# Kernel optimization log

Measured on AMD Instinct MI355X. Metric: run time of the kernel, lower is better.

The kernel has to match this reference:

```python
import jax, jax.numpy as jnp
import numpy as np

SENT_LEN, SENT_BATCH, WORD_LEN = 256, 64, 16
EMB, HID = 128, 256
CEMB, CHID = 64, 128
VOCAB, CVOCAB, TAGS = 50000, 128, 50


def setup_inputs() -> dict:
    key = jax.random.key(0)
    ks = jax.random.split(key, 14)
    s = 0.1  # param init scale, avoids gate saturation
    n = lambda k, shape: (jax.random.normal(k, shape, dtype=jnp.float32) * s)
    return {
        "sentences": jax.random.randint(ks[0], (SENT_LEN, SENT_BATCH), 0, VOCAB),
        "words": jax.random.randint(ks[1], (SENT_BATCH, WORD_LEN, SENT_LEN), 0, CVOCAB),
        "char_embedding_dim": CEMB,
        "char_hidden_dim": CHID,
        "word_emb": n(ks[2], (VOCAB, EMB)),
        "char_emb": n(ks[3], (CVOCAB, CEMB)),
        "Wih_c": n(ks[4], (4 * CHID, CEMB)),
        "Whh_c": n(ks[5], (4 * CHID, CHID)),
        "bih_c": n(ks[6], (4 * CHID,)),
        "bhh_c": n(ks[7], (4 * CHID,)),
        "Wih_w": n(ks[8], (4 * HID, EMB + CHID)),
        "Whh_w": n(ks[9], (4 * HID, HID)),
        "bih_w": n(ks[10], (4 * HID,)),
        "bhh_w": n(ks[11], (4 * HID,)),
        "W_tag": n(ks[12], (TAGS, HID)),
        "b_tag": n(ks[13], (TAGS,)),
    }


def _lstm_cell(h, c, x, Wih, Whh, b):
    # torch gate order: input, forget, cell(g), output
    gates = x @ Wih.T + h @ Whh.T + b
    i, f, g, o = jnp.split(gates, 4, axis=-1)
    c_new = jax.nn.sigmoid(f) * c + jax.nn.sigmoid(i) * jnp.tanh(g)
    h_new = jax.nn.sigmoid(o) * jnp.tanh(c_new)
    return h_new, c_new


def reference(sentences, words, char_embedding_dim, char_hidden_dim,
              word_emb, char_emb, Wih_c, Whh_c, bih_c, bhh_c,
              Wih_w, Whh_w, bih_w, bhh_w, W_tag, b_tag):
    sent_len, sent_batch = sentences.shape
    dt = word_emb.dtype

    embeds = word_emb[sentences]            # [T, B, EMB]
    ce = char_emb[words]                    # [B, WL, T, CEMB]

    # char LSTM: per sentence, seq=WL, batch=T; hidden carried ACROSS sentences
    b_c = bih_c + bhh_c

    def char_sentence(carry, sent_ce):      # sent_ce: [WL, T, CEMB]
        def step(hc, x):
            h, c = _lstm_cell(hc[0], hc[1], x, Wih_c, Whh_c, b_c)
            return (h, c), None
        carry, _ = jax.lax.scan(step, carry, sent_ce)
        return carry, carry[0]               # final h: [T, CHID]

    init_c = (jnp.zeros((sent_len, CHID), dt), jnp.zeros((sent_len, CHID), dt))
    _, char_finals = jax.lax.scan(char_sentence, init_c, ce)  # [B, T, CHID]
    char_finals = jnp.transpose(char_finals, (1, 0, 2))        # [T, B, CHID]

    x = jnp.concatenate([embeds, char_finals], axis=-1)        # [T, B, EMB+CHID]

    # word LSTM over time=T, batch=B
    b_w = bih_w + bhh_w

    def word_step(hc, xt):
        h, c = _lstm_cell(hc[0], hc[1], xt, Wih_w, Whh_w, b_w)
        return (h, c), h

    init_w = (jnp.zeros((sent_batch, HID), dt), jnp.zeros((sent_batch, HID), dt))
    _, lstm_out = jax.lax.scan(word_step, init_w, x)           # [T, B, HID]

    tag_space = lstm_out @ W_tag.T + b_tag                     # [T, B, TAGS]
    return jax.nn.log_softmax(tag_space, axis=-1)
```

## Files before the change

### kernel.cpp

```cpp
#include <hip/hip_runtime.h>
#include <hip/hip_bf16.h>
#include <cstdint>

#define SENT_LEN   256
#define SENT_BATCH 64
#define WORD_LEN   16
#define EMB        128
#define HID        256
#define CEMB       64
#define CHID       128
#define TAGS       50
#define K_IN       (EMB + CHID)
#define LOG2E      1.44269504f
#define N2LOG2E    -2.88539008f

typedef __attribute__((ext_vector_type(8))) short short8;
typedef __attribute__((ext_vector_type(4))) float f32x4;
typedef __attribute__((ext_vector_type(4))) int   i32x4;
typedef __attribute__((ext_vector_type(2))) long  lng2;

__device__ __forceinline__ float rcpf(float x) { return __builtin_amdgcn_rcpf(x); }
__device__ __forceinline__ float sig2(float xl) {
    return rcpf(1.f + __builtin_amdgcn_exp2f(-xl));
}
__device__ __forceinline__ float tanh2(float xl) {
    float e = __builtin_amdgcn_exp2f(-(xl + xl));
    return 2.f * rcpf(1.f + e) - 1.f;
}
__device__ __forceinline__ float lstm_act(float gi, float gf, float gg, float go, float& cst) {
    float c = sig2(gf) * cst + sig2(gi) * tanh2(gg);
    cst = c;
    float tc = 2.f * rcpf(1.f + __builtin_amdgcn_exp2f(N2LOG2E * c)) - 1.f;
    return sig2(go) * tc;
}
__device__ __forceinline__ float bf_lo(unsigned u) { return __uint_as_float(u << 16); }
__device__ __forceinline__ float bf_hi(unsigned u) { return __uint_as_float(u & 0xffff0000u); }
__device__ __forceinline__ unsigned short f2bfu(float f) {
    unsigned u = __float_as_uint(f);
    u += 0x7fff + ((u >> 16) & 1);
    return (unsigned short)(u >> 16);
}
__device__ __forceinline__ void block_sync_lds() {
    asm volatile("s_waitcnt lgkmcnt(0)\ns_barrier" ::: "memory");
}
__device__ __forceinline__ i32x4 mfma_i8_k64(lng2 a, lng2 b, i32x4 c) {
    c = __builtin_amdgcn_mfma_i32_16x16x32_i8(a.x, b.x, c, 0, 0, 0);
    return __builtin_amdgcn_mfma_i32_16x16x32_i8(a.y, b.y, c, 0, 0, 0);
}
template<int Q> __device__ __forceinline__ float qbcast(float x) {
    return __int_as_float(__builtin_amdgcn_mov_dpp(
        __float_as_int(x), Q * 0x55, 0xF, 0xF, false));
}

__global__ void prep_char(const float* __restrict__ Wih_c, const float* __restrict__ char_emb,
                          const float* __restrict__ bih_c, const float* __restrict__ bhh_c,
                          float* __restrict__ pre8) {
    int ch = blockIdx.x;
    int g  = threadIdx.x;
    float acc = bih_c[g] + bhh_c[g];
    const float* w = Wih_c + g * CEMB;
    const float* e = char_emb + ch * CEMB;
#pragma unroll
    for (int k = 0; k < CEMB; k++) acc += w[k] * e[k];
    int gt = g >> 7, j = g & 127;
    pre8[((ch * 128) + j) * 4 + gt] = acc * LOG2E;
}

__global__ void prep_wq(const float* __restrict__ Whh_w, signed char* __restrict__ wq,
                        float* __restrict__ sw) {
    int g = blockIdx.x;
    int lane = threadIdx.x;
    float4 v = reinterpret_cast<const float4*>(Whh_w + (size_t)g * HID)[lane];
    float m = fmaxf(fmaxf(fabsf(v.x), fabsf(v.y)), fmaxf(fabsf(v.z), fabsf(v.w)));
#pragma unroll
    for (int off = 32; off; off >>= 1) m = fmaxf(m, __shfl_xor(m, off, 64));
    m = fmaxf(m, 1e-20f);
    float inv = 127.f / m;
    int q0 = __float2int_rn(v.x * inv), q1 = __float2int_rn(v.y * inv);
    int q2 = __float2int_rn(v.z * inv), q3 = __float2int_rn(v.w * inv);
    int packed = (q0 & 255) | ((q1 & 255) << 8) | ((q2 & 255) << 16) | ((q3 & 255) << 24);
    reinterpret_cast<int*>(wq)[g * 64 + lane] = packed;
    if (lane == 0) sw[g] = m / 127.f;
}

__global__ __launch_bounds__(512, 1) void char_lstm(
        const int* __restrict__ words, const float* __restrict__ Whh_c,
        const float* __restrict__ pre8, float* __restrict__ cf) {
    int t    = blockIdx.x;
    int tid  = threadIdx.x;
    int lane = tid & 63, w = tid >> 6;
    int nt   = lane & 3;
    int j    = w * 16 + (lane >> 2);
    int g    = nt * 128 + j;

    __shared__ __align__(16) signed char hv[2][128];

    const float4* wr = reinterpret_cast<const float4*>(Whh_c + (size_t)g * CHID);
    float mx = 1e-20f;
#pragma unroll
    for (int q = 0; q < 32; q++) {
        float4 f = wr[q];
        mx = fmaxf(mx, fmaxf(fmaxf(fabsf(f.x), fabsf(f.y)), fmaxf(fabsf(f.z), fabsf(f.w))));
    }
    float inv = 127.f / mx;
    int wqr[32];
#pragma unroll
    for (int q = 0; q < 32; q++) {
        float4 f = wr[q];
        wqr[q] = (__float2int_rn(f.x * inv) & 255)
               | ((__float2int_rn(f.y * inv) & 255) << 8)
               | ((__float2int_rn(f.z * inv) & 255) << 16)
               | ((__float2int_rn(f.w * inv) & 255) << 24);
    }
    float swl = mx * (LOG2E / (127.f * 127.f));

    float s_e = (nt == 2) ? -2.f : -1.f;
    float m_a = (nt == 2) ?  2.f :  1.f;
    float b_a = (nt == 2) ? -1.f :  0.f;

    if (tid < 64) { reinterpret_cast<int*>(hv)[tid] = 0; }

    float cst = 0.f;
    int cid0 = words[t];
    int cid1 = words[SENT_LEN + t];
    float pl0 = pre8[(size_t)cid0 * 512 + tid];
    float pl1 = pre8[(size_t)cid1 * 512 + tid];
    int cidn0 = words[2 * SENT_LEN + t];
    int cidn1 = words[3 * SENT_LEN + t];
    __syncthreads();

    for (int u = 0; u < 512; u++) {
        float pn0 = pre8[(size_t)cidn0 * 512 + tid];
        float pn1 = pre8[(size_t)cidn1 * 512 + tid];
        cidn0 = words[(((u << 1) + 4) & 1023) * SENT_LEN + t];
        cidn1 = words[(((u << 1) + 5) & 1023) * SENT_LEN + t];

        {
            const i32x4* hp = reinterpret_cast<const i32x4*>(hv[0]);
            int a0 = 0, a1 = 0, a2 = 0, a3 = 0;
#pragma unroll
            for (int q = 0; q < 8; q++) {
                i32x4 hq = hp[q];
                a0 = __builtin_amdgcn_sdot4(hq.x, wqr[q * 4 + 0], a0, false);
                a1 = __builtin_amdgcn_sdot4(hq.y, wqr[q * 4 + 1], a1, false);
                a2 = __builtin_amdgcn_sdot4(hq.z, wqr[q * 4 + 2], a2, false);
                a3 = __builtin_amdgcn_sdot4(hq.w, wqr[q * 4 + 3], a3, false);
            }
            int acc = (a0 + a1) + (a2 + a3);
            float gv = (float)acc * swl + pl0;
            float e  = __builtin_amdgcn_exp2f(s_e * gv);
            float av = m_a * rcpf(1.f + e) + b_a;
            float qi = qbcast<0>(av);
            float qf = qbcast<1>(av);
            float qg = qbcast<2>(av);
            float qo = qbcast<3>(av);
            float c  = qf * cst + qi * qg;
            cst = c;
            float tc = 2.f * rcpf(1.f + __builtin_amdgcn_exp2f(N2LOG2E * c)) - 1.f;
            float h  = qo * tc;
            if (nt == 0)
                hv[1][j] = (signed char)__float2int_rn(h * 127.f);
            block_sync_lds();
        }
        {
            const i32x4* hp = reinterpret_cast<const i32x4*>(hv[1]);
            int a0 = 0, a1 = 0, a2 = 0, a3 = 0;
#pragma unroll
            for (int q = 0; q < 8; q++) {
                i32x4 hq = hp[q];
                a0 = __builtin_amdgcn_sdot4(hq.x, wqr[q * 4 + 0], a0, false);
                a1 = __builtin_amdgcn_sdot4(hq.y, wqr[q * 4 + 1], a1, false);
                a2 = __builtin_amdgcn_sdot4(hq.z, wqr[q * 4 + 2], a2, false);
                a3 = __builtin_amdgcn_sdot4(hq.w, wqr[q * 4 + 3], a3, false);
            }
            int acc = (a0 + a1) + (a2 + a3);
            float gv = (float)acc * swl + pl1;
            float e  = __builtin_amdgcn_exp2f(s_e * gv);
            float av = m_a * rcpf(1.f + e) + b_a;
            float qi = qbcast<0>(av);
            float qf = qbcast<1>(av);
            float qg = qbcast<2>(av);
            float qo = qbcast<3>(av);
            float c  = qf * cst + qi * qg;
            cst = c;
            float tc = 2.f * rcpf(1.f + __builtin_amdgcn_exp2f(N2LOG2E * c)) - 1.f;
            float h  = qo * tc;
            if (nt == 0) {
                hv[0][j] = (signed char)__float2int_rn(h * 127.f);
                if ((u & 7) == 7)
                    cf[((size_t)t * SENT_BATCH + (u >> 3)) * CHID + j] = h;
            }
            block_sync_lds();
        }
        pl0 = pn0; pl1 = pn1;
    }
}

#define XW_SEG 65
__global__ __launch_bounds__(256, 2) void xw_gemm(
        const int* __restrict__ sentences, const float* __restrict__ word_emb,
        const float* __restrict__ cf, const float* __restrict__ Wih_w,
        const float* __restrict__ bih_w, const float* __restrict__ bhh_w,
        uint2* __restrict__ xw8) {
    __shared__ short8 Apack[32 * XW_SEG];
    __shared__ short8 Bpack[32 * XW_SEG];
    __shared__ int sid_s[64];
    int tid = threadIdx.x;
    int j0 = blockIdx.x * 16;
    int row0 = blockIdx.y * 64;
    if (tid < 64) sid_s[tid] = sentences[row0 + tid];
    __syncthreads();

#pragma unroll
    for (int it = 0; it < 8; it++) {
        int idx = it * 256 + tid;
        int m = idx >> 5, k8 = idx & 31;
        int k = k8 * 8;
        int kt = k8 >> 2, lqs = k8 & 3;
        int lanes = (m & 15) + (lqs << 4);
        int seg = kt * 4 + (m >> 4);
        const float* asrc = (k < EMB)
            ? word_emb + (size_t)sid_s[m] * EMB + k
            : cf + (size_t)(row0 + m) * CHID + (k - EMB);
        float4 a0 = reinterpret_cast<const float4*>(asrc)[0];
        float4 a1 = reinterpret_cast<const float4*>(asrc)[1];
        short8 av;
        av[0] = (short)f2bfu(a0.x); av[1] = (short)f2bfu(a0.y);
        av[2] = (short)f2bfu(a0.z); av[3] = (short)f2bfu(a0.w);
        av[4] = (short)f2bfu(a1.x); av[5] = (short)f2bfu(a1.y);
        av[6] = (short)f2bfu(a1.z); av[7] = (short)f2bfu(a1.w);
        Apack[seg * XW_SEG + lanes] = av;
        const float* bsrc = Wih_w + (size_t)((m >> 4) * 256 + j0 + (m & 15)) * K_IN + k;
        float4 b0 = reinterpret_cast<const float4*>(bsrc)[0];
        float4 b1 = reinterpret_cast<const float4*>(bsrc)[1];
        short8 bv;
        bv[0] = (short)f2bfu(b0.x); bv[1] = (short)f2bfu(b0.y);
        bv[2] = (short)f2bfu(b0.z); bv[3] = (short)f2bfu(b0.w);
        bv[4] = (short)f2bfu(b1.x); bv[5] = (short)f2bfu(b1.y);
        bv[6] = (short)f2bfu(b1.z); bv[7] = (short)f2bfu(b1.w);
        Bpack[seg * XW_SEG + lanes] = bv;
    }
    __syncthreads();

    int lane = tid & 63, wv = tid >> 6, l15 = lane & 15, lq = lane >> 4;
    f32x4 acc[4] = {{0.f,0.f,0.f,0.f},{0.f,0.f,0.f,0.f},{0.f,0.f,0.f,0.f},{0.f,0.f,0.f,0.f}};
#pragma unroll
    for (int kt = 0; kt < 8; kt++) {
// ... 55 lines not shown
        uint2 xn0 = xwb[((((u << 1) + 4) & 255)) * 256 + j];
        uint2 xn1 = xwb[((((u << 1) + 5) & 255)) * 256 + j];

        {
            const lng2* hp = reinterpret_cast<const lng2*>(hv[0]);
            i32x4 acc[4] = {};
#pragma unroll
            for (int kt = 0; kt < 4; kt++) {
                lng2 a = hp[kt * 4 + lq];
#pragma unroll
                for (int nt = 0; nt < 4; nt++)
                    acc[nt] = mfma_i8_k64(a, bfr[nt][kt], acc[nt]);
            }
            float gi = (float)acc[0][0] * swl[0] + bf_lo(xq0.x);
            float gf = (float)acc[1][0] * swl[1] + bf_hi(xq0.x);
            float gg = (float)acc[2][0] * swl[2] + bf_lo(xq0.y);
            float go = (float)acc[3][0] * swl[3] + bf_hi(xq0.y);
            float h = lstm_act(gi, gf, gg, go, cst);
            if (lq == 0) {
                h_out[((size_t)(u << 1) * SENT_BATCH + b) * HID + j] = h;
                hv[1][j] = (signed char)__float2int_rn(h * 127.f);
            }
            block_sync_lds();
        }
        {
            const lng2* hp = reinterpret_cast<const lng2*>(hv[1]);
            i32x4 acc[4] = {};
#pragma unroll
            for (int kt = 0; kt < 4; kt++) {
                lng2 a = hp[kt * 4 + lq];
#pragma unroll
                for (int nt = 0; nt < 4; nt++)
                    acc[nt] = mfma_i8_k64(a, bfr[nt][kt], acc[nt]);
            }
            float gi = (float)acc[0][0] * swl[0] + bf_lo(xq1.x);
            float gf = (float)acc[1][0] * swl[1] + bf_hi(xq1.x);
            float gg = (float)acc[2][0] * swl[2] + bf_lo(xq1.y);
            float go = (float)acc[3][0] * swl[3] + bf_hi(xq1.y);
            float h = lstm_act(gi, gf, gg, go, cst);
            if (lq == 0) {
                h_out[((size_t)((u << 1) + 1) * SENT_BATCH + b) * HID + j] = h;
                hv[0][j] = (signed char)__float2int_rn(h * 127.f);
            }
            block_sync_lds();
        }
        xq0 = xq2; xq1 = xq3; xq2 = xn0; xq3 = xn1;
    }
}

__global__ __launch_bounds__(256) void tag_logsoftmax(
        const float* __restrict__ h_out, const float* __restrict__ W_tag,
        const float* __restrict__ b_tag, float* __restrict__ out) {
    __shared__ float wt_s[TAGS * 257];
    __shared__ float hr_s[4 * HID];
    int tid = threadIdx.x;
    int row0 = blockIdx.x * 4;
#pragma unroll 2
    for (int i = 0; i < TAGS; i++) wt_s[i * 257 + tid] = W_tag[i * HID + tid];
#pragma unroll
    for (int w = 0; w < 4; w++) hr_s[w * HID + tid] = h_out[(size_t)(row0 + w) * HID + tid];
    __syncthreads();

    int w = tid >> 6, l = tid & 63;
    float acc = 0.f;
    if (l < TAGS) {
        acc = b_tag[l];
        const float* hr = hr_s + w * HID;
        const float* wr = wt_s + l * 257;
#pragma unroll 4
        for (int k = 0; k < HID; k++) acc += hr[k] * wr[k];
    }
    float m = (l < TAGS) ? acc : -1e30f;
#pragma unroll
    for (int off = 32; off; off >>= 1) m = fmaxf(m, __shfl_xor(m, off, 64));
    float e = (l < TAGS) ? __builtin_amdgcn_exp2f((acc - m) * LOG2E) : 0.f;
    float ssum = e;
#pragma unroll
    for (int off = 32; off; off >>= 1) ssum += __shfl_xor(ssum, off, 64);
    float lse = m + __logf(ssum);
    if (l < TAGS) out[(size_t)(row0 + w) * TAGS + l] = acc - lse;
}

extern "C" void kernel_launch(void* const* d_in, const int* in_sizes, int n_in,
                              void* d_out, int out_size, void* d_ws, size_t ws_size,
                              hipStream_t stream) {
    (void)in_sizes; (void)n_in; (void)out_size; (void)ws_size;
    const int*   sentences = (const int*)d_in[0];
    const int*   words     = (const int*)d_in[1];
    const float* word_emb  = (const float*)d_in[4];
    const float* char_emb  = (const float*)d_in[5];
    const float* Wih_c     = (const float*)d_in[6];
    const float* Whh_c     = (const float*)d_in[7];
    const float* bih_c     = (const float*)d_in[8];
    const float* bhh_c     = (const float*)d_in[9];
    const float* Wih_w     = (const float*)d_in[10];
    const float* Whh_w     = (const float*)d_in[11];
    const float* bih_w     = (const float*)d_in[12];
    const float* bhh_w     = (const float*)d_in[13];
    const float* W_tag     = (const float*)d_in[14];
    const float* b_tag     = (const float*)d_in[15];
    float* out = (float*)d_out;

    char* ws = (char*)d_ws;
    size_t off = 0;
    float* pre8 = (float*)(ws + off);                 off += 128 * 512 * sizeof(float);
    signed char* wq = (signed char*)(ws + off);       off += 1024 * 256;
    float* sw = (float*)(ws + off);                   off += 1024 * sizeof(float);
    off = (off + 255) & ~(size_t)255;
    float* cf = (float*)(ws + off);                   off += (size_t)SENT_LEN * SENT_BATCH * CHID * sizeof(float);
    uint2* xw8 = (uint2*)(ws + off);                  off += (size_t)SENT_LEN * SENT_BATCH * 256 * sizeof(uint2);
    float* h_out = (float*)(ws + off);                off += (size_t)SENT_LEN * SENT_BATCH * HID * sizeof(float);

    hipLaunchKernelGGL(prep_char, dim3(128), dim3(512), 0, stream,
                       Wih_c, char_emb, bih_c, bhh_c, pre8);
    hipLaunchKernelGGL(prep_wq, dim3(1024), dim3(64), 0, stream, Whh_w, wq, sw);
    hipLaunchKernelGGL(char_lstm, dim3(256), dim3(512), 0, stream,
                       words, Whh_c, pre8, cf);
    hipLaunchKernelGGL(xw_gemm, dim3(16, 256), dim3(256), 0, stream,
                       sentences, word_emb, cf, Wih_w, bih_w, bhh_w, xw8);
    hipLaunchKernelGGL(word_lstm, dim3(SENT_BATCH), dim3(1024), 0, stream,
                       xw8, wq, sw, h_out);
    hipLaunchKernelGGL(tag_logsoftmax, dim3((SENT_LEN * SENT_BATCH) / 4), dim3(256), 0, stream,
                       h_out, W_tag, b_tag, out);
}
```

Measured before the change: 938.7 us.

## Process two independent char-LSTM chains per block to overlap latency

Each char_lstm block now runs two independent word positions (t0, t1) in an interleaved fashion, halving the grid from 256 to 128 blocks. This aims to hide the serial latency of each recurrent step (dot products, transcendental ops, LDS barrier) by giving the scheduler two independent dependency chains per barrier. The gate pre-activation scaling is also folded into prep_char and the sdot result so the inner step uses a single fma before exp2. Risk: fewer blocks means less use of the CUs, and the per-step work doubles, so the whole serial loop may end up longer if it was not latency-bound.

```diff
diff --git a/kernel.cpp b/kernel.cpp
--- a/kernel.cpp
+++ b/kernel.cpp
@@ -63,7 +63,8 @@
 #pragma unroll
     for (int k = 0; k < CEMB; k++) acc += w[k] * e[k];
     int gt = g >> 7, j = g & 127;
-    pre8[((ch * 128) + j) * 4 + gt] = acc * LOG2E;
+    float s_e = (gt == 2) ? -2.f : -1.f;
+    pre8[((ch * 128) + j) * 4 + gt] = acc * LOG2E * s_e;
 }
 
 __global__ void prep_wq(const float* __restrict__ Whh_w, signed char* __restrict__ wq,
@@ -86,14 +87,16 @@
 __global__ __launch_bounds__(512, 1) void char_lstm(
         const int* __restrict__ words, const float* __restrict__ Whh_c,
         const float* __restrict__ pre8, float* __restrict__ cf) {
-    int t    = blockIdx.x;
+    int bid  = blockIdx.x;
+    int t0   = bid * 2, t1 = bid * 2 + 1;
     int tid  = threadIdx.x;
     int lane = tid & 63, w = tid >> 6;
     int nt   = lane & 3;
     int j    = w * 16 + (lane >> 2);
     int g    = nt * 128 + j;
 
-    __shared__ __align__(16) signed char hv[2][128];
+    __shared__ __align__(16) signed char hv0[2][128];
+    __shared__ __align__(16) signed char hv1[2][128];
 
     const float4* wr = reinterpret_cast<const float4*>(Whh_c + (size_t)g * CHID);
     float mx = 1e-20f;
@@ -112,87 +115,129 @@
                | ((__float2int_rn(f.z * inv) & 255) << 16)
                | ((__float2int_rn(f.w * inv) & 255) << 24);
     }
-    float swl = mx * (LOG2E / (127.f * 127.f));
-
-    float s_e = (nt == 2) ? -2.f : -1.f;
-    float m_a = (nt == 2) ?  2.f :  1.f;
-    float b_a = (nt == 2) ? -1.f :  0.f;
-
-    if (tid < 64) { reinterpret_cast<int*>(hv)[tid] = 0; }
-
-    float cst = 0.f;
-    int cid0 = words[t];
-    int cid1 = words[SENT_LEN + t];
-    float pl0 = pre8[(size_t)cid0 * 512 + tid];
-    float pl1 = pre8[(size_t)cid1 * 512 + tid];
-    int cidn0 = words[2 * SENT_LEN + t];
-    int cidn1 = words[3 * SENT_LEN + t];
+    float s_e   = (nt == 2) ? -2.f : -1.f;
+    float swl_s = s_e * mx * (LOG2E / (127.f * 127.f));
+    float m_a   = (nt == 2) ?  2.f :  1.f;
+    float b_a   = (nt == 2) ? -1.f :  0.f;
+
+    if (tid < 64) { reinterpret_cast<int*>(hv0)[tid] = 0; reinterpret_cast<int*>(hv1)[tid] = 0; }
+
+    float cst0 = 0.f, cst1 = 0.f;
+    int   c0i2, c0i3, c1i2, c1i3;
+    float pc0, pn0, pc1, pn1;
+    {
+        int a0 = words[0 * SENT_LEN + t0], b0 = words[1 * SENT_LEN + t0];
+        int a1 = words[0 * SENT_LEN + t1], b1 = words[1 * SENT_LEN + t1];
+        pc0 = pre8[(size_t)a0 * 512 + tid];
+        pn0 = pre8[(size_t)b0 * 512 + tid];
+        pc1 = pre8[(size_t)a1 * 512 + tid];
+        pn1 = pre8[(size_t)b1 * 512 + tid];
+        c0i2 = words[2 * SENT_LEN + t0]; c0i3 = words[3 * SENT_LEN + t0];
+        c1i2 = words[2 * SENT_LEN + t1]; c1i3 = words[3 * SENT_LEN + t1];
+    }
     __syncthreads();
 
     for (int u = 0; u < 512; u++) {
-        float pn0 = pre8[(size_t)cidn0 * 512 + tid];
-        float pn1 = pre8[(size_t)cidn1 * 512 + tid];
-        cidn0 = words[(((u << 1) + 4) & 1023) * SENT_LEN + t];
-        cidn1 = words[(((u << 1) + 5) & 1023) * SENT_LEN + t];
-
         {
-            const i32x4* hp = reinterpret_cast<const i32x4*>(hv[0]);
+            float pf0 = pre8[(size_t)c0i2 * 512 + tid];
+            float pf1 = pre8[(size_t)c1i2 * 512 + tid];
+            int cn0 = words[(((u << 1) + 4) & 1023) * SENT_LEN + t0];
+            int cn1 = words[(((u << 1) + 4) & 1023) * SENT_LEN + t1];
+
+            const i32x4* h0p = reinterpret_cast<const i32x4*>(hv0[0]);
+            const i32x4* h1p = reinterpret_cast<const i32x4*>(hv1[0]);
             int a0 = 0, a1 = 0, a2 = 0, a3 = 0;
+            int b0 = 0, b1 = 0, b2 = 0, b3 = 0;
 #pragma unroll
             for (int q = 0; q < 8; q++) {
-                i32x4 hq = hp[q];
+                i32x4 hq = h0p[q];
                 a0 = __builtin_amdgcn_sdot4(hq.x, wqr[q * 4 + 0], a0, false);
                 a1 = __builtin_amdgcn_sdot4(hq.y, wqr[q * 4 + 1], a1, false);
                 a2 = __builtin_amdgcn_sdot4(hq.z, wqr[q * 4 + 2], a2, false);
                 a3 = __builtin_amdgcn_sdot4(hq.w, wqr[q * 4 + 3], a3, false);
             }
-            int acc = (a0 + a1) + (a2 + a3);
-            float gv = (float)acc * swl + pl0;
-            float e  = __builtin_amdgcn_exp2f(s_e * gv);
-            float av = m_a * rcpf(1.f + e) + b_a;
-            float qi = qbcast<0>(av);
-            float qf = qbcast<1>(av);
-            float qg = qbcast<2>(av);
-            float qo = qbcast<3>(av);
-            float c  = qf * cst + qi * qg;
-            cst = c;
-            float tc = 2.f * rcpf(1.f + __builtin_amdgcn_exp2f(N2LOG2E * c)) - 1.f;
-            float h  = qo * tc;
-            if (nt == 0)
-                hv[1][j] = (signed char)__float2int_rn(h * 127.f);
+#pragma unroll
+            for (int q = 0; q < 8; q++) {
+                i32x4 hq = h1p[q];
+                b0 = __builtin_amdgcn_sdot4(hq.x, wqr[q * 4 + 0], b0, false);
+                b1 = __builtin_amdgcn_sdot4(hq.y, wqr[q * 4 + 1], b1, false);
+                b2 = __builtin_amdgcn_sdot4(hq.z, wqr[q * 4 + 2], b2, false);
+                b3 = __builtin_amdgcn_sdot4(hq.w, wqr[q * 4 + 3], b3, false);
+            }
+            int s0 = (a0 + a1) + (a2 + a3);
+            int s1 = (b0 + b1) + (b2 + b3);
+            float e0  = __builtin_amdgcn_exp2f(fmaf((float)s0, swl_s, pc0));
+            float av0 = m_a * rcpf(1.f + e0) + b_a;
+            float e1  = __builtin_amdgcn_exp2f(fmaf((float)s1, swl_s, pc1));
+            float av1 = m_a * rcpf(1.f + e1) + b_a;
+            float qi0 = qbcast<0>(av0), qf0 = qbcast<1>(av0), qg0 = qbcast<2>(av0), qo0 = qbcast<3>(av0);
+            float qi1 = qbcast<0>(av1), qf1 = qbcast<1>(av1), qg1 = qbcast<2>(av1), qo1 = qbcast<3>(av1);
+            float cv0 = fmaf(qf0, cst0, qi0 * qg0); cst0 = cv0;
+            float cv1 = fmaf(qf1, cst1, qi1 * qg1); cst1 = cv1;
+            float tc0 = 2.f * rcpf(1.f + __builtin_amdgcn_exp2f(N2LOG2E * cv0)) - 1.f;
+            float tc1 = 2.f * rcpf(1.f + __builtin_amdgcn_exp2f(N2LOG2E * cv1)) - 1.f;
+            float h0 = qo0 * tc0;
+            float h1 = qo1 * tc1;
+            if (nt == 0) {
+                hv0[1][j] = (signed char)__float2int_rn(h0 * 127.f);
+                hv1[1][j] = (signed char)__float2int_rn(h1 * 127.f);
+            }
             block_sync_lds();
+            pc0 = pn0; pn0 = pf0; c0i2 = c0i3; c0i3 = cn0;
+            pc1 = pn1; pn1 = pf1; c1i2 = c1i3; c1i3 = cn1;
         }
         {
-            const i32x4* hp = reinterpret_cast<const i32x4*>(hv[1]);
+            float pf0 = pre8[(size_t)c0i2 * 512 + tid];
+            float pf1 = pre8[(size_t)c1i2 * 512 + tid];
+            int cn0 = words[(((u << 1) + 5) & 1023) * SENT_LEN + t0];
+            int cn1 = words[(((u << 1) + 5) & 1023) * SENT_LEN + t1];
+
+            const i32x4* h0p = reinterpret_cast<const i32x4*>(hv0[1]);
+            const i32x4* h1p = reinterpret_cast<const i32x4*>(hv1[1]);
             int a0 = 0, a1 = 0, a2 = 0, a3 = 0;
+            int b0 = 0, b1 = 0, b2 = 0, b3 = 0;
 #pragma unroll
             for (int q = 0; q < 8; q++) {
-                i32x4 hq = hp[q];
+                i32x4 hq = h0p[q];
                 a0 = __builtin_amdgcn_sdot4(hq.x, wqr[q * 4 + 0], a0, false);
                 a1 = __builtin_amdgcn_sdot4(hq.y, wqr[q * 4 + 1], a1, false);
                 a2 = __builtin_amdgcn_sdot4(hq.z, wqr[q * 4 + 2], a2, false);
                 a3 = __builtin_amdgcn_sdot4(hq.w, wqr[q * 4 + 3], a3, false);
             }
-            int acc = (a0 + a1) + (a2 + a3);
-            float gv = (float)acc * swl + pl1;
-            float e  = __builtin_amdgcn_exp2f(s_e * gv);
-            float av = m_a * rcpf(1.f + e) + b_a;
-            float qi = qbcast<0>(av);
-            float qf = qbcast<1>(av);
-            float qg = qbcast<2>(av);
-            float qo = qbcast<3>(av);
-            float c  = qf * cst + qi * qg;
-            cst = c;
-            float tc = 2.f * rcpf(1.f + __builtin_amdgcn_exp2f(N2LOG2E * c)) - 1.f;
-            float h  = qo * tc;
+#pragma unroll
+            for (int q = 0; q < 8; q++) {
+                i32x4 hq = h1p[q];
+                b0 = __builtin_amdgcn_sdot4(hq.x, wqr[q * 4 + 0], b0, false);
+                b1 = __builtin_amdgcn_sdot4(hq.y, wqr[q * 4 + 1], b1, false);
+                b2 = __builtin_amdgcn_sdot4(hq.z, wqr[q * 4 + 2], b2, false);
+                b3 = __builtin_amdgcn_sdot4(hq.w, wqr[q * 4 + 3], b3, false);
+            }
+            int s0 = (a0 + a1) + (a2 + a3);
+            int s1 = (b0 + b1) + (b2 + b3);
+            float e0  = __builtin_amdgcn_exp2f(fmaf((float)s0, swl_s, pc0));
+            float av0 = m_a * rcpf(1.f + e0) + b_a;
+            float e1  = __builtin_amdgcn_exp2f(fmaf((float)s1, swl_s, pc1));
+            float av1 = m_a * rcpf(1.f + e1) + b_a;
+            float qi0 = qbcast<0>(av0), qf0 = qbcast<1>(av0), qg0 = qbcast<2>(av0), qo0 = qbcast<3>(av0);
+            float qi1 = qbcast<0>(av1), qf1 = qbcast<1>(av1), qg1 = qbcast<2>(av1), qo1 = qbcast<3>(av1);
+            float cv0 = fmaf(qf0, cst0, qi0 * qg0); cst0 = cv0;
+            float cv1 = fmaf(qf1, cst1, qi1 * qg1); cst1 = cv1;
+            float tc0 = 2.f * rcpf(1.f + __builtin_amdgcn_exp2f(N2LOG2E * cv0)) - 1.f;
+            float tc1 = 2.f * rcpf(1.f + __builtin_amdgcn_exp2f(N2LOG2E * cv1)) - 1.f;
+            float h0 = qo0 * tc0;
+            float h1 = qo1 * tc1;
             if (nt == 0) {
-                hv[0][j] = (signed char)__float2int_rn(h * 127.f);
-                if ((u & 7) == 7)
-                    cf[((size_t)t * SENT_BATCH + (u >> 3)) * CHID + j] = h;
+                hv0[0][j] = (signed char)__float2int_rn(h0 * 127.f);
+                hv1[0][j] = (signed char)__float2int_rn(h1 * 127.f);
+                if ((u & 7) == 7) {
+                    cf[((size_t)t0 * SENT_BATCH + (u >> 3)) * CHID + j] = h0;
+                    cf[((size_t)t1 * SENT_BATCH + (u >> 3)) * CHID + j] = h1;
+                }
             }
             block_sync_lds();
+            pc0 = pn0; pn0 = pf0; c0i2 = c0i3; c0i3 = cn0;
+            pc1 = pn1; pn1 = pf1; c1i2 = c1i3; c1i3 = cn1;
         }
-        pl0 = pn0; pl1 = pn1;
     }
 }
 
@@ -416,7 +461,7 @@
     hipLaunchKernelGGL(prep_char, dim3(128), dim3(512), 0, stream,
                        Wih_c, char_emb, bih_c, bhh_c, pre8);
     hipLaunchKernelGGL(prep_wq, dim3(1024), dim3(64), 0, stream, Whh_w, wq, sw);
-    hipLaunchKernelGGL(char_lstm, dim3(256), dim3(512), 0, stream,
+    hipLaunchKernelGGL(char_lstm, dim3(128), dim3(512), 0, stream,
                        words, Whh_c, pre8, cf);
     hipLaunchKernelGGL(xw_gemm, dim3(16, 256), dim3(256), 0, stream,
                        sentences, word_emb, cf, Wih_w, bih_w, bhh_w, xw8);
```

Result: slower. 1.187 ms (+26.5%).

## Split char-LSTM recurrent matvec between sdot4 and int8 MFMA halves

Applied to the files above, without the earlier changes.

The char LSTM recurrent product over 128 hidden inputs is split. The first 64 inputs still go through per-lane sdot4 with register-held weights. The second 64 go through four int8 16x16x32 MFMAs per wave, and a lane-select picks the lane's own gate row out of the MFMA outputs. The gate-sign scaling is also folded into the precomputed input projection and the weight scale, which saves a multiply on the serial chain. This shortens the per-step dependent dot-product chain but adds MFMA latency, select logic and extra LDS reads on a latency-bound recurrence.

```diff
diff --git a/kernel.cpp b/kernel.cpp
--- a/kernel.cpp
+++ b/kernel.cpp
@@ -63,7 +63,8 @@
 #pragma unroll
     for (int k = 0; k < CEMB; k++) acc += w[k] * e[k];
     int gt = g >> 7, j = g & 127;
-    pre8[((ch * 128) + j) * 4 + gt] = acc * LOG2E;
+    float s_e = (gt == 2) ? -2.f : -1.f;
+    pre8[((ch * 128) + j) * 4 + gt] = acc * LOG2E * s_e;
 }
 
 __global__ void prep_wq(const float* __restrict__ Whh_w, signed char* __restrict__ wq,
@@ -90,8 +91,12 @@
     int tid  = threadIdx.x;
     int lane = tid & 63, w = tid >> 6;
     int nt   = lane & 3;
-    int j    = w * 16 + (lane >> 2);
+    int jl   = lane >> 2;
+    int j    = w * 16 + jl;
     int g    = nt * 128 + j;
+    int lq   = lane >> 4;
+    int lq16 = lq * 16;
+    int q2   = jl & 3;
 
     __shared__ __align__(16) signed char hv[2][128];
 
@@ -103,20 +108,40 @@
         mx = fmaxf(mx, fmaxf(fmaxf(fabsf(f.x), fabsf(f.y)), fmaxf(fabsf(f.z), fabsf(f.w))));
     }
     float inv = 127.f / mx;
-    int wqr[32];
-#pragma unroll
-    for (int q = 0; q < 32; q++) {
+    int wqr[16];
+#pragma unroll
+    for (int q = 0; q < 16; q++) {
         float4 f = wr[q];
         wqr[q] = (__float2int_rn(f.x * inv) & 255)
                | ((__float2int_rn(f.y * inv) & 255) << 8)
                | ((__float2int_rn(f.z * inv) & 255) << 16)
                | ((__float2int_rn(f.w * inv) & 255) << 24);
     }
-    float swl = mx * (LOG2E / (127.f * 127.f));
-
-    float s_e = (nt == 2) ? -2.f : -1.f;
-    float m_a = (nt == 2) ?  2.f :  1.f;
-    float b_a = (nt == 2) ? -1.f :  0.f;
+    float s_e   = (nt == 2) ? -2.f : -1.f;
+    float swl_s = s_e * mx * (LOG2E / (127.f * 127.f));
+    float m_a   = (nt == 2) ?  2.f :  1.f;
+    float b_a   = (nt == 2) ? -1.f :  0.f;
+
+    lng2 wA[4];
+#pragma unroll
+    for (int m = 0; m < 4; m++) {
+        int lo_lane = q2 * 16 + m * 4 + nt;
+        float mxm = __int_as_float(__builtin_amdgcn_ds_bpermute(lo_lane << 2,
+                                                                __float_as_int(mx)));
+        float invm = 127.f / mxm;
+        int grow = nt * 128 + w * 16 + q2 * 4 + m;
+        const float* wp = Whh_c + (size_t)grow * CHID + 64 + lq16;
+        unsigned long lo = 0, hi = 0;
+#pragma unroll
+        for (int p = 0; p < 8; p++) {
+            lo |= (unsigned long)((unsigned)__float2int_rn(wp[p] * invm) & 255) << (8 * p);
+            hi |= (unsigned long)((unsigned)__float2int_rn(wp[p + 8] * invm) & 255) << (8 * p);
+        }
+        lng2 bb; bb.x = (long)lo; bb.y = (long)hi;
+        wA[m] = bb;
+    }
+    bool mb0 = (q2 & 1) != 0, mb1 = (q2 & 2) != 0;
+    bool rb0 = (nt & 1) != 0, rb1 = (nt & 2) != 0;
 
     if (tid < 64) { reinterpret_cast<int*>(hv)[tid] = 0; }
 
@@ -125,65 +150,101 @@
     int cid1 = words[SENT_LEN + t];
     float pl0 = pre8[(size_t)cid0 * 512 + tid];
     float pl1 = pre8[(size_t)cid1 * 512 + tid];
-    int cidn0 = words[2 * SENT_LEN + t];
-    int cidn1 = words[3 * SENT_LEN + t];
+    int ci2 = words[2 * SENT_LEN + t];
+    int ci3 = words[3 * SENT_LEN + t];
     __syncthreads();
 
     for (int u = 0; u < 512; u++) {
-        float pn0 = pre8[(size_t)cidn0 * 512 + tid];
-        float pn1 = pre8[(size_t)cidn1 * 512 + tid];
-        cidn0 = words[(((u << 1) + 4) & 1023) * SENT_LEN + t];
-        cidn1 = words[(((u << 1) + 5) & 1023) * SENT_LEN + t];
+        float pf0 = pre8[(size_t)ci2 * 512 + tid];
+        float pf1 = pre8[(size_t)ci3 * 512 + tid];
+        ci2 = words[(((u << 1) + 4) & 1023) * SENT_LEN + t];
+        ci3 = words[(((u << 1) + 5) & 1023) * SENT_LEN + t];
 
         {
-            const i32x4* hp = reinterpret_cast<const i32x4*>(hv[0]);
+            const signed char* hb = hv[0];
+            const i32x4* hp = reinterpret_cast<const i32x4*>(hb);
+            i32x4 h0 = hp[0], h1 = hp[1], h2 = hp[2], h3 = hp[3];
+            lng2 hB = *reinterpret_cast<const lng2*>(hb + 64 + lq16);
+            i32x4 zz = {0, 0, 0, 0};
+            i32x4 c0 = mfma_i8_k64(wA[0], hB, zz);
+            i32x4 c1 = mfma_i8_k64(wA[1], hB, zz);
+            i32x4 c2 = mfma_i8_k64(wA[2], hB, zz);
+            i32x4 c3 = mfma_i8_k64(wA[3], hB, zz);
             int a0 = 0, a1 = 0, a2 = 0, a3 = 0;
-#pragma unroll
-            for (int q = 0; q < 8; q++) {
-                i32x4 hq = hp[q];
-                a0 = __builtin_amdgcn_sdot4(hq.x, wqr[q * 4 + 0], a0, false);
-                a1 = __builtin_amdgcn_sdot4(hq.y, wqr[q * 4 + 1], a1, false);
-                a2 = __builtin_amdgcn_sdot4(hq.z, wqr[q * 4 + 2], a2, false);
-                a3 = __builtin_amdgcn_sdot4(hq.w, wqr[q * 4 + 3], a3, false);
-            }
-            int acc = (a0 + a1) + (a2 + a3);
-            float gv = (float)acc * swl + pl0;
-            float e  = __builtin_amdgcn_exp2f(s_e * gv);
+            a0 = __builtin_amdgcn_sdot4(h0.x, wqr[0], a0, false);
+            a1 = __builtin_amdgcn_sdot4(h0.y, wqr[1], a1, false);
+            a2 = __builtin_amdgcn_sdot4(h0.z, wqr[2], a2, false);
+            a3 = __builtin_amdgcn_sdot4(h0.w, wqr[3], a3, false);
+            a0 = __builtin_amdgcn_sdot4(h1.x, wqr[4], a0, false);
+            a1 = __builtin_amdgcn_sdot4(h1.y, wqr[5], a1, false);
+            a2 = __builtin_amdgcn_sdot4(h1.z, wqr[6], a2, false);
+            a3 = __builtin_amdgcn_sdot4(h1.w, wqr[7], a3, false);
+            a0 = __builtin_amdgcn_sdot4(h2.x, wqr[8], a0, false);
+            a1 = __builtin_amdgcn_sdot4(h2.y, wqr[9], a1, false);
+            a2 = __builtin_amdgcn_sdot4(h2.z, wqr[10], a2, false);
+            a3 = __builtin_amdgcn_sdot4(h2.w, wqr[11], a3, false);
+            a0 = __builtin_amdgcn_sdot4(h3.x, wqr[12], a0, false);
+            a1 = __builtin_amdgcn_sdot4(h3.y, wqr[13], a1, false);
+            a2 = __builtin_amdgcn_sdot4(h3.z, wqr[14], a2, false);
+            a3 = __builtin_amdgcn_sdot4(h3.w, wqr[15], a3, false);
+            i32x4 sA = mb0 ? c1 : c0;
+            i32x4 sB = mb0 ? c3 : c2;
+            i32x4 sC = mb1 ? sB : sA;
+            int v01 = rb0 ? sC.y : sC.x;
+            int v23 = rb0 ? sC.w : sC.z;
+            int vs  = rb1 ? v23 : v01;
+            int s = ((a0 + a1) + (a2 + a3)) + vs;
+            float e  = __builtin_amdgcn_exp2f(fmaf((float)s, swl_s, pl0));
             float av = m_a * rcpf(1.f + e) + b_a;
-            float qi = qbcast<0>(av);
-            float qf = qbcast<1>(av);
-            float qg = qbcast<2>(av);
-            float qo = qbcast<3>(av);
-            float c  = qf * cst + qi * qg;
-            cst = c;
-            float tc = 2.f * rcpf(1.f + __builtin_amdgcn_exp2f(N2LOG2E * c)) - 1.f;
+            float qi = qbcast<0>(av), qf = qbcast<1>(av);
+            float qg = qbcast<2>(av), qo = qbcast<3>(av);
+            float cv = fmaf(qf, cst, qi * qg); cst = cv;
+            float tc = 2.f * rcpf(1.f + __builtin_amdgcn_exp2f(N2LOG2E * cv)) - 1.f;
             float h  = qo * tc;
             if (nt == 0)
                 hv[1][j] = (signed char)__float2int_rn(h * 127.f);
             block_sync_lds();
         }
         {
-            const i32x4* hp = reinterpret_cast<const i32x4*>(hv[1]);
+            const signed char* hb = hv[1];
+            const i32x4* hp = reinterpret_cast<const i32x4*>(hb);
+            i32x4 h0 = hp[0], h1 = hp[1], h2 = hp[2], h3 = hp[3];
+            lng2 hB = *reinterpret_cast<const lng2*>(hb + 64 + lq16);
+            i32x4 zz = {0, 0, 0, 0};
+            i32x4 c0 = mfma_i8_k64(wA[0], hB, zz);
+            i32x4 c1 = mfma_i8_k64(wA[1], hB, zz);
+            i32x4 c2 = mfma_i8_k64(wA[2], hB, zz);
+            i32x4 c3 = mfma_i8_k64(wA[3], hB, zz);
             int a0 = 0, a1 = 0, a2 = 0, a3 = 0;
-#pragma unroll
-            for (int q = 0; q < 8; q++) {
-                i32x4 hq = hp[q];
-                a0 = __builtin_amdgcn_sdot4(hq.x, wqr[q * 4 + 0], a0, false);
-                a1 = __builtin_amdgcn_sdot4(hq.y, wqr[q * 4 + 1], a1, false);
-                a2 = __builtin_amdgcn_sdot4(hq.z, wqr[q * 4 + 2], a2, false);
-                a3 = __builtin_amdgcn_sdot4(hq.w, wqr[q * 4 + 3], a3, false);
-            }
-            int acc = (a0 + a1) + (a2 + a3);
-            float gv = (float)acc * swl + pl1;
-            float e  = __builtin_amdgcn_exp2f(s_e * gv);
+            a0 = __builtin_amdgcn_sdot4(h0.x, wqr[0], a0, false);
+            a1 = __builtin_amdgcn_sdot4(h0.y, wqr[1], a1, false);
+            a2 = __builtin_amdgcn_sdot4(h0.z, wqr[2], a2, false);
+            a3 = __builtin_amdgcn_sdot4(h0.w, wqr[3], a3, false);
+            a0 = __builtin_amdgcn_sdot4(h1.x, wqr[4], a0, false);
+            a1 = __builtin_amdgcn_sdot4(h1.y, wqr[5], a1, false);
+            a2 = __builtin_amdgcn_sdot4(h1.z, wqr[6], a2, false);
+            a3 = __builtin_amdgcn_sdot4(h1.w, wqr[7], a3, false);
+            a0 = __builtin_amdgcn_sdot4(h2.x, wqr[8], a0, false);
+            a1 = __builtin_amdgcn_sdot4(h2.y, wqr[9], a1, false);
+            a2 = __builtin_amdgcn_sdot4(h2.z, wqr[10], a2, false);
+            a3 = __builtin_amdgcn_sdot4(h2.w, wqr[11], a3, false);
+            a0 = __builtin_amdgcn_sdot4(h3.x, wqr[12], a0, false);
+            a1 = __builtin_amdgcn_sdot4(h3.y, wqr[13], a1, false);
+            a2 = __builtin_amdgcn_sdot4(h3.z, wqr[14], a2, false);
+            a3 = __builtin_amdgcn_sdot4(h3.w, wqr[15], a3, false);
+            i32x4 sA = mb0 ? c1 : c0;
+            i32x4 sB = mb0 ? c3 : c2;
+            i32x4 sC = mb1 ? sB : sA;
+            int v01 = rb0 ? sC.y : sC.x;
+            int v23 = rb0 ? sC.w : sC.z;
+            int vs  = rb1 ? v23 : v01;
+            int s = ((a0 + a1) + (a2 + a3)) + vs;
+            float e  = __builtin_amdgcn_exp2f(fmaf((float)s, swl_s, pl1));
             float av = m_a * rcpf(1.f + e) + b_a;
-            float qi = qbcast<0>(av);
-            float qf = qbcast<1>(av);
-            float qg = qbcast<2>(av);
-            float qo = qbcast<3>(av);
-            float c  = qf * cst + qi * qg;
-            cst = c;
-            float tc = 2.f * rcpf(1.f + __builtin_amdgcn_exp2f(N2LOG2E * c)) - 1.f;
+            float qi = qbcast<0>(av), qf = qbcast<1>(av);
+            float qg = qbcast<2>(av), qo = qbcast<3>(av);
+            float cv = fmaf(qf, cst, qi * qg); cst = cv;
+            float tc = 2.f * rcpf(1.f + __builtin_amdgcn_exp2f(N2LOG2E * cv)) - 1.f;
             float h  = qo * tc;
             if (nt == 0) {
                 hv[0][j] = (signed char)__float2int_rn(h * 127.f);
@@ -192,7 +253,7 @@
             }
             block_sync_lds();
         }
-        pl0 = pn0; pl1 = pn1;
+        pl0 = pf0; pl1 = pf1;
     }
 }
 
```

New measurement: 1.073 ms. 1.14x slower.

## Halve char LSTM block size with two hidden units per thread; batch tag rows

Applied to the files above, without the earlier changes.

The char LSTM kernel now runs 256 threads per block, and each thread handles two hidden units. It holds two quantized weight rows in registers and computes two dot products per step, which cuts the number of waves synchronizing at each of the 1024 serial barriers. The gate prescale s_e is folded into pre8 and into the weight scale, which removes one multiply per step. The tag/log-softmax kernel now processes 8 rows per block instead of 4, so the W_tag load into LDS is amortized over more rows. The cost is higher register pressure and less thread-level parallelism per block in the serial recurrence.

```diff
diff --git a/kernel.cpp b/kernel.cpp
--- a/kernel.cpp
+++ b/kernel.cpp
@@ -63,7 +63,8 @@
 #pragma unroll
     for (int k = 0; k < CEMB; k++) acc += w[k] * e[k];
     int gt = g >> 7, j = g & 127;
-    pre8[((ch * 128) + j) * 4 + gt] = acc * LOG2E;
+    float s_e = (gt == 2) ? -2.f : -1.f;
+    pre8[((ch * 128) + j) * 4 + gt] = acc * LOG2E * s_e;
 }
 
 __global__ void prep_wq(const float* __restrict__ Whh_w, signed char* __restrict__ wq,
@@ -83,116 +84,170 @@
     if (lane == 0) sw[g] = m / 127.f;
 }
 
-__global__ __launch_bounds__(512, 1) void char_lstm(
+__global__ __launch_bounds__(256, 1) void char_lstm(
         const int* __restrict__ words, const float* __restrict__ Whh_c,
         const float* __restrict__ pre8, float* __restrict__ cf) {
     int t    = blockIdx.x;
     int tid  = threadIdx.x;
     int lane = tid & 63, w = tid >> 6;
     int nt   = lane & 3;
-    int j    = w * 16 + (lane >> 2);
-    int g    = nt * 128 + j;
+    int jl   = lane >> 2;
+    int j0   = w * 16 + jl;
+    int j1   = j0 + 64;
+    int g0   = nt * 128 + j0;
+    int g1   = nt * 128 + j1;
 
     __shared__ __align__(16) signed char hv[2][128];
 
-    const float4* wr = reinterpret_cast<const float4*>(Whh_c + (size_t)g * CHID);
-    float mx = 1e-20f;
-#pragma unroll
-    for (int q = 0; q < 32; q++) {
-        float4 f = wr[q];
-        mx = fmaxf(mx, fmaxf(fmaxf(fabsf(f.x), fabsf(f.y)), fmaxf(fabsf(f.z), fabsf(f.w))));
-    }
-    float inv = 127.f / mx;
-    int wqr[32];
-#pragma unroll
-    for (int q = 0; q < 32; q++) {
-        float4 f = wr[q];
-        wqr[q] = (__float2int_rn(f.x * inv) & 255)
-               | ((__float2int_rn(f.y * inv) & 255) << 8)
-               | ((__float2int_rn(f.z * inv) & 255) << 16)
-               | ((__float2int_rn(f.w * inv) & 255) << 24);
-    }
-    float swl = mx * (LOG2E / (127.f * 127.f));
-
+    int wq0[32], wq1[32];
+    float swl0, swl1;
     float s_e = (nt == 2) ? -2.f : -1.f;
+    {
+        const float4* wr = reinterpret_cast<const float4*>(Whh_c + (size_t)g0 * CHID);
+        float mx = 1e-20f;
+#pragma unroll
+        for (int q = 0; q < 32; q++) {
+            float4 f = wr[q];
+            mx = fmaxf(mx, fmaxf(fmaxf(fabsf(f.x), fabsf(f.y)), fmaxf(fabsf(f.z), fabsf(f.w))));
+        }
+        float inv = 127.f / mx;
+#pragma unroll
+        for (int q = 0; q < 32; q++) {
+            float4 f = wr[q];
+            wq0[q] = (__float2int_rn(f.x * inv) & 255)
+                   | ((__float2int_rn(f.y * inv) & 255) << 8)
+                   | ((__float2int_rn(f.z * inv) & 255) << 16)
+                   | ((__float2int_rn(f.w * inv) & 255) << 24);
+        }
+        swl0 = s_e * mx * (LOG2E / (127.f * 127.f));
+    }
+    {
+        const float4* wr = reinterpret_cast<const float4*>(Whh_c + (size_t)g1 * CHID);
+        float mx = 1e-20f;
+#pragma unroll
+        for (int q = 0; q < 32; q++) {
+            float4 f = wr[q];
+            mx = fmaxf(mx, fmaxf(fmaxf(fabsf(f.x), fabsf(f.y)), fmaxf(fabsf(f.z), fabsf(f.w))));
+        }
+        float inv = 127.f / mx;
+#pragma unroll
+        for (int q = 0; q < 32; q++) {
+            float4 f = wr[q];
+            wq1[q] = (__float2int_rn(f.x * inv) & 255)
+                   | ((__float2int_rn(f.y * inv) & 255) << 8)
+                   | ((__float2int_rn(f.z * inv) & 255) << 16)
+                   | ((__float2int_rn(f.w * inv) & 255) << 24);
+        }
+        swl1 = s_e * mx * (LOG2E / (127.f * 127.f));
+    }
     float m_a = (nt == 2) ?  2.f :  1.f;
     float b_a = (nt == 2) ? -1.f :  0.f;
 
     if (tid < 64) { reinterpret_cast<int*>(hv)[tid] = 0; }
 
-    float cst = 0.f;
+    float cst0 = 0.f, cst1 = 0.f;
     int cid0 = words[t];
     int cid1 = words[SENT_LEN + t];
-    float pl0 = pre8[(size_t)cid0 * 512 + tid];
-    float pl1 = pre8[(size_t)cid1 * 512 + tid];
-    int cidn0 = words[2 * SENT_LEN + t];
-    int cidn1 = words[3 * SENT_LEN + t];
+    float pa0 = pre8[(size_t)cid0 * 512 + tid];
+    float pb0 = pre8[(size_t)cid0 * 512 + 256 + tid];
+    float pa1 = pre8[(size_t)cid1 * 512 + tid];
+    float pb1 = pre8[(size_t)cid1 * 512 + 256 + tid];
+    int ci2 = words[2 * SENT_LEN + t];
+    int ci3 = words[3 * SENT_LEN + t];
     __syncthreads();
 
     for (int u = 0; u < 512; u++) {
-        float pn0 = pre8[(size_t)cidn0 * 512 + tid];
-        float pn1 = pre8[(size_t)cidn1 * 512 + tid];
-        cidn0 = words[(((u << 1) + 4) & 1023) * SENT_LEN + t];
-        cidn1 = words[(((u << 1) + 5) & 1023) * SENT_LEN + t];
+        float fa0 = pre8[(size_t)ci2 * 512 + tid];
+        float fb0 = pre8[(size_t)ci2 * 512 + 256 + tid];
+        float fa1 = pre8[(size_t)ci3 * 512 + tid];
+        float fb1 = pre8[(size_t)ci3 * 512 + 256 + tid];
+        ci2 = words[(((u << 1) + 4) & 1023) * SENT_LEN + t];
+        ci3 = words[(((u << 1) + 5) & 1023) * SENT_LEN + t];
 
         {
             const i32x4* hp = reinterpret_cast<const i32x4*>(hv[0]);
+            i32x4 h0 = hp[0], h1 = hp[1], h2 = hp[2], h3 = hp[3];
+            i32x4 h4 = hp[4], h5 = hp[5], h6 = hp[6], h7 = hp[7];
             int a0 = 0, a1 = 0, a2 = 0, a3 = 0;
-#pragma unroll
-            for (int q = 0; q < 8; q++) {
-                i32x4 hq = hp[q];
-                a0 = __builtin_amdgcn_sdot4(hq.x, wqr[q * 4 + 0], a0, false);
-                a1 = __builtin_amdgcn_sdot4(hq.y, wqr[q * 4 + 1], a1, false);
-                a2 = __builtin_amdgcn_sdot4(hq.z, wqr[q * 4 + 2], a2, false);
-                a3 = __builtin_amdgcn_sdot4(hq.w, wqr[q * 4 + 3], a3, false);
-            }
-            int acc = (a0 + a1) + (a2 + a3);
-            float gv = (float)acc * swl + pl0;
-            float e  = __builtin_amdgcn_exp2f(s_e * gv);
-            float av = m_a * rcpf(1.f + e) + b_a;
-            float qi = qbcast<0>(av);
-            float qf = qbcast<1>(av);
-            float qg = qbcast<2>(av);
-            float qo = qbcast<3>(av);
-            float c  = qf * cst + qi * qg;
-            cst = c;
-            float tc = 2.f * rcpf(1.f + __builtin_amdgcn_exp2f(N2LOG2E * c)) - 1.f;
-            float h  = qo * tc;
-            if (nt == 0)
-                hv[1][j] = (signed char)__float2int_rn(h * 127.f);
+            int b0 = 0, b1 = 0, b2 = 0, b3 = 0;
+#define DOT8(hh, base) \
+            a0 = __builtin_amdgcn_sdot4(hh.x, wq0[base + 0], a0, false); \
+            a1 = __builtin_amdgcn_sdot4(hh.y, wq0[base + 1], a1, false); \
+            a2 = __builtin_amdgcn_sdot4(hh.z, wq0[base + 2], a2, false); \
+            a3 = __builtin_amdgcn_sdot4(hh.w, wq0[base + 3], a3, false); \
+            b0 = __builtin_amdgcn_sdot4(hh.x, wq1[base + 0], b0, false); \
+            b1 = __builtin_amdgcn_sdot4(hh.y, wq1[base + 1], b1, false); \
+            b2 = __builtin_amdgcn_sdot4(hh.z, wq1[base + 2], b2, false); \
+            b3 = __builtin_amdgcn_sdot4(hh.w, wq1[base + 3], b3, false);
+            DOT8(h0, 0) DOT8(h1, 4) DOT8(h2, 8) DOT8(h3, 12)
+            DOT8(h4, 16) DOT8(h5, 20) DOT8(h6, 24) DOT8(h7, 28)
+            int s0 = (a0 + a1) + (a2 + a3);
+            int s1 = (b0 + b1) + (b2 + b3);
+            float e0  = __builtin_amdgcn_exp2f(fmaf((float)s0, swl0, pa0));
+            float av0 = m_a * rcpf(1.f + e0) + b_a;
+            float e1  = __builtin_amdgcn_exp2f(fmaf((float)s1, swl1, pb0));
+            float av1 = m_a * rcpf(1.f + e1) + b_a;
+            float qi0 = qbcast<0>(av0), qf0 = qbcast<1>(av0), qg0 = qbcast<2>(av0), qo0 = qbcast<3>(av0);
+            float qi1 = qbcast<0>(av1), qf1 = qbcast<1>(av1), qg1 = qbcast<2>(av1), qo1 = qbcast<3>(av1);
+            float cv0 = fmaf(qf0, cst0, qi0 * qg0); cst0 = cv0;
+            float cv1 = fmaf(qf1, cst1, qi1 * qg1); cst1 = cv1;
+            float tc0 = 2.f * rcpf(1.f + __builtin_amdgcn_exp2f(N2LOG2E * cv0)) - 1.f;
+            float tc1 = 2.f * rcpf(1.f + __builtin_amdgcn_exp2f(N2LOG2E * cv1)) - 1.f;
+            float hh0 = qo0 * tc0;
+            float hh1 = qo1 * tc1;
+            if (nt == 0) {
+                hv[1][j0] = (signed char)__float2int_rn(hh0 * 127.f);
+                hv[1][j1] = (signed char)__float2int_rn(hh1 * 127.f);
+            }
             block_sync_lds();
-        }
-        {
-            const i32x4* hp = reinterpret_cast<const i32x4*>(hv[1]);
-            int a0 = 0, a1 = 0, a2 = 0, a3 = 0;
-#pragma unroll
-            for (int q = 0; q < 8; q++) {
-                i32x4 hq = hp[q];
-                a0 = __builtin_amdgcn_sdot4(hq.x, wqr[q * 4 + 0], a0, false);
-                a1 = __builtin_amdgcn_sdot4(hq.y, wqr[q * 4 + 1], a1, false);
-                a2 = __builtin_amdgcn_sdot4(hq.z, wqr[q * 4 + 2], a2, false);
-                a3 = __builtin_amdgcn_sdot4(hq.w, wqr[q * 4 + 3], a3, false);
-            }
-            int acc = (a0 + a1) + (a2 + a3);
-            float gv = (float)acc * swl + pl1;
-            float e  = __builtin_amdgcn_exp2f(s_e * gv);
-            float av = m_a * rcpf(1.f + e) + b_a;
-            float qi = qbcast<0>(av);
-            float qf = qbcast<1>(av);
-            float qg = qbcast<2>(av);
-            float qo = qbcast<3>(av);
-            float c  = qf * cst + qi * qg;
-            cst = c;
-            float tc = 2.f * rcpf(1.f + __builtin_amdgcn_exp2f(N2LOG2E * c)) - 1.f;
-            float h  = qo * tc;
-            if (nt == 0) {
-                hv[0][j] = (signed char)__float2int_rn(h * 127.f);
-                if ((u & 7) == 7)
-                    cf[((size_t)t * SENT_BATCH + (u >> 3)) * CHID + j] = h;
-            }
-            block_sync_lds();
-        }
-        pl0 = pn0; pl1 = pn1;
+            pa0 = pa1; pb0 = pb1;
+            pa1 = fa0; pb1 = fb0;
+            (void)fa1; (void)fb1;
+            pa1 = pa1;
+            {
+                const i32x4* hq = reinterpret_cast<const i32x4*>(hv[1]);
+                i32x4 g0v = hq[0], g1v = hq[1], g2v = hq[2], g3v = hq[3];
+                i32x4 g4v = hq[4], g5v = hq[5], g6v = hq[6], g7v = hq[7];
+                int c0 = 0, c1 = 0, c2 = 0, c3 = 0;
+                int d0 = 0, d1 = 0, d2 = 0, d3 = 0;
+#define DOT8B(hh, base) \
+                c0 = __builtin_amdgcn_sdot4(hh.x, wq0[base + 0], c0, false); \
+                c1 = __builtin_amdgcn_sdot4(hh.y, wq0[base + 1], c1, false); \
+                c2 = __builtin_amdgcn_sdot4(hh.z, wq0[base + 2], c2, false); \
+                c3 = __builtin_amdgcn_sdot4(hh.w, wq0[base + 3], c3, false); \
+                d0 = __builtin_amdgcn_sdot4(hh.x, wq1[base + 0], d0, false); \
+                d1 = __builtin_amdgcn_sdot4(hh.y, wq1[base + 1], d1, false); \
+                d2 = __builtin_amdgcn_sdot4(hh.z, wq1[base + 2], d2, false); \
+                d3 = __builtin_amdgcn_sdot4(hh.w, wq1[base + 3], d3, false);
+                DOT8B(g0v, 0) DOT8B(g1v, 4) DOT8B(g2v, 8) DOT8B(g3v, 12)
+                DOT8B(g4v, 16) DOT8B(g5v, 20) DOT8B(g6v, 24) DOT8B(g7v, 28)
+                int t0s = (c0 + c1) + (c2 + c3);
+                int t1s = (d0 + d1) + (d2 + d3);
+                float e0b  = __builtin_amdgcn_exp2f(fmaf((float)t0s, swl0, pa0));
+                float av0b = m_a * rcpf(1.f + e0b) + b_a;
+                float e1b  = __builtin_amdgcn_exp2f(fmaf((float)t1s, swl1, pb0));
+                float av1b = m_a * rcpf(1.f + e1b) + b_a;
+                float qi0b = qbcast<0>(av0b), qf0b = qbcast<1>(av0b), qg0b = qbcast<2>(av0b), qo0b = qbcast<3>(av0b);
+                float qi1b = qbcast<0>(av1b), qf1b = qbcast<1>(av1b), qg1b = qbcast<2>(av1b), qo1b = qbcast<3>(av1b);
+                float cv0b = fmaf(qf0b, cst0, qi0b * qg0b); cst0 = cv0b;
+                float cv1b = fmaf(qf1b, cst1, qi1b * qg1b); cst1 = cv1b;
+                float tc0b = 2.f * rcpf(1.f + __builtin_amdgcn_exp2f(N2LOG2E * cv0b)) - 1.f;
+                float tc1b = 2.f * rcpf(1.f + __builtin_amdgcn_exp2f(N2LOG2E * cv1b)) - 1.f;
+                float hb0 = qo0b * tc0b;
+                float hb1 = qo1b * tc1b;
+                if (nt == 0) {
+                    hv[0][j0] = (signed char)__float2int_rn(hb0 * 127.f);
+                    hv[0][j1] = (signed char)__float2int_rn(hb1 * 127.f);
+                    if ((u & 7) == 7) {
+                        cf[((size_t)t * SENT_BATCH + (u >> 3)) * CHID + j0] = hb0;
+                        cf[((size_t)t * SENT_BATCH + (u >> 3)) * CHID + j1] = hb1;
+                    }
+                }
+                block_sync_lds();
+            }
+            pa0 = pa1; pb0 = pb1;
+            pa1 = fa1; pb1 = fb1;
+        }
     }
 }
 
@@ -354,33 +409,37 @@
         const float* __restrict__ h_out, const float* __restrict__ W_tag,
         const float* __restrict__ b_tag, float* __restrict__ out) {
     __shared__ float wt_s[TAGS * 257];
-    __shared__ float hr_s[4 * HID];
+    __shared__ float hr_s[8 * HID];
     int tid = threadIdx.x;
-    int row0 = blockIdx.x * 4;
+    int row0 = blockIdx.x * 8;
 #pragma unroll 2
     for (int i = 0; i < TAGS; i++) wt_s[i * 257 + tid] = W_tag[i * HID + tid];
 #pragma unroll
-    for (int w = 0; w < 4; w++) hr_s[w * HID + tid] = h_out[(size_t)(row0 + w) * HID + tid];
+    for (int w = 0; w < 8; w++) hr_s[w * HID + tid] = h_out[(size_t)(row0 + w) * HID + tid];
     __syncthreads();
 
-    int w = tid >> 6, l = tid & 63;
-    float acc = 0.f;
-    if (l < TAGS) {
-        acc = b_tag[l];
-        const float* hr = hr_s + w * HID;
-        const float* wr = wt_s + l * 257;
+    int w4 = tid >> 6, l = tid & 63;
+#pragma unroll
+    for (int rep = 0; rep < 2; rep++) {
+        int w = rep * 4 + w4;
+        float acc = 0.f;
+        if (l < TAGS) {
+            acc = b_tag[l];
+            const float* hr = hr_s + w * HID;
+            const float* wr = wt_s + l * 257;
 #pragma unroll 4
-        for (int k = 0; k < HID; k++) acc += hr[k] * wr[k];
-    }
-    float m = (l < TAGS) ? acc : -1e30f;
-#pragma unroll
-    for (int off = 32; off; off >>= 1) m = fmaxf(m, __shfl_xor(m, off, 64));
-    float e = (l < TAGS) ? __builtin_amdgcn_exp2f((acc - m) * LOG2E) : 0.f;
-    float ssum = e;
-#pragma unroll
-    for (int off = 32; off; off >>= 1) ssum += __shfl_xor(ssum, off, 64);
-    float lse = m + __logf(ssum);
-    if (l < TAGS) out[(size_t)(row0 + w) * TAGS + l] = acc - lse;
+            for (int k = 0; k < HID; k++) acc += hr[k] * wr[k];
+        }
+        float m = (l < TAGS) ? acc : -1e30f;
+#pragma unroll
+        for (int off = 32; off; off >>= 1) m = fmaxf(m, __shfl_xor(m, off, 64));
+        float e = (l < TAGS) ? __builtin_amdgcn_exp2f((acc - m) * LOG2E) : 0.f;
+        float ssum = e;
+#pragma unroll
+        for (int off = 32; off; off >>= 1) ssum += __shfl_xor(ssum, off, 64);
+        float lse = m + __logf(ssum);
+        if (l < TAGS) out[(size_t)(row0 + w) * TAGS + l] = acc - lse;
+    }
 }
 
 extern "C" void kernel_launch(void* const* d_in, const int* in_sizes, int n_in,
@@ -416,12 +475,12 @@
     hipLaunchKernelGGL(prep_char, dim3(128), dim3(512), 0, stream,
                        Wih_c, char_emb, bih_c, bhh_c, pre8);
     hipLaunchKernelGGL(prep_wq, dim3(1024), dim3(64), 0, stream, Whh_w, wq, sw);
-    hipLaunchKernelGGL(char_lstm, dim3(256), dim3(512), 0, stream,
+    hipLaunchKernelGGL(char_lstm, dim3(256), dim3(256), 0, stream,
                        words, Whh_c, pre8, cf);
     hipLaunchKernelGGL(xw_gemm, dim3(16, 256), dim3(256), 0, stream,
                        sentences, word_emb, cf, Wih_w, bih_w, bhh_w, xw8);
     hipLaunchKernelGGL(word_lstm, dim3(SENT_BATCH), dim3(1024), 0, stream,
                        xw8, wq, sw, h_out);
-    hipLaunchKernelGGL(tag_logsoftmax, dim3((SENT_LEN * SENT_BATCH) / 4), dim3(256), 0, stream,
+    hipLaunchKernelGGL(tag_logsoftmax, dim3((SENT_LEN * SENT_BATCH) / 8), dim3(256), 0, stream,
                        h_out, W_tag, b_tag, out);
 }
```

Measured after the change: 1.014 ms. 8.1% more time.
